# Kernel tuning notes

Hardware: AMD Instinct MI355X
Metric: run time of the kernel (lower is better)

The kernel has to match this reference:

```python
import jax, jax.numpy as jnp
import numpy as np

HIDDEN = 1024
BATCH = 32
SRC_LEN = 4096


def setup_inputs() -> dict:
    key = jax.random.key(0)
    k1, k2, k3, k4, k5 = jax.random.split(key, 5)
    query = jax.random.normal(k1, (BATCH, HIDDEN), dtype=jnp.float32)
    keys = jax.random.normal(k2, (BATCH, SRC_LEN, HIDDEN), dtype=jnp.float32)
    values = jax.random.normal(k3, (BATCH, SRC_LEN, HIDDEN), dtype=jnp.float32)
    mask = jax.random.randint(k4, (BATCH, SRC_LEN), 0, 2).astype(jnp.bool_)
    # nn.Linear(hidden, hidden, bias=False): y = x @ W.T, W: (out, in)
    W = jax.random.normal(k5, (HIDDEN, HIDDEN), dtype=jnp.float32) / np.sqrt(HIDDEN)
    return {"query": query, "keys": keys, "values": values, "mask": mask, "W": W}


def reference(query, keys, values, mask, W):
    # proj_query = linear_in(query): (b, h)
    proj_query = query @ W.T
    # scores = bmm(keys, proj_query[:, :, None]).squeeze: (b, s)
    scores = jnp.einsum("bsh,bh->bs", keys, proj_query)
    scores = jnp.where(mask, -jnp.inf, scores)
    attn_weights = jax.nn.softmax(scores, axis=-1)  # (b, s)
    # context = bmm(attn[:, None, :], values).squeeze: (b, h)
    context = jnp.einsum("bs,bsh->bh", attn_weights, values)
    return (context, attn_weights)
```

## Files before the change

kernel.cpp:

```cpp
#include <hip/hip_runtime.h>

constexpr int HIDDEN = 1024;
constexpr int BATCH  = 32;
constexpr int SRC    = 4096;
constexpr int CHUNK  = 128;
constexpr int NCHUNK = SRC / CHUNK;
constexpr int KSPLIT = 4;

#define NEG_INF (-__builtin_inff())


typedef float floatx4 __attribute__((ext_vector_type(4)));

__device__ __forceinline__ float4 ntload4(const float4* p) {
    floatx4 v = __builtin_nontemporal_load((const floatx4*)p);
    return make_float4(v.x, v.y, v.z, v.w);
}

__device__ __forceinline__ float wave_reduce_add(float v) {
    #pragma unroll
    for (int off = 32; off > 0; off >>= 1)
        v += __shfl_down(v, off, 64);
    return v;
}

__device__ __forceinline__ float wave_reduce_max(float v) {
    #pragma unroll
    for (int off = 32; off > 0; off >>= 1)
        v = fmaxf(v, __shfl_down(v, off, 64));
    return v;
}

__device__ __forceinline__ float dot16(float4 a, float4 b, float4 c, float4 d,
                                       float4 q0, float4 q1, float4 q2, float4 q3) {
    return a.x*q0.x + a.y*q0.y + a.z*q0.z + a.w*q0.w
         + b.x*q1.x + b.y*q1.y + b.z*q1.z + b.w*q1.w
         + c.x*q2.x + c.y*q2.y + c.z*q2.z + c.w*q2.w
         + d.x*q3.x + d.y*q3.y + d.z*q3.z + d.w*q3.w;
}

__global__ __launch_bounds__(256) void k_proj(const float* __restrict__ query,
                                              const float* __restrict__ W,
                                              float* __restrict__ pproj) {
    int g = blockIdx.x * 256 + threadIdx.x;
    int b = g & (BATCH - 1);
    int o = g >> 5;
    int z = blockIdx.y;
    const float4* W4 = (const float4*)(W + (size_t)o * HIDDEN) + z * (HIDDEN / 4 / KSPLIT);
    const float4* Q4 = (const float4*)(query + (size_t)b * HIDDEN) + z * (HIDDEN / 4 / KSPLIT);
    float4 acc = {0.f, 0.f, 0.f, 0.f};
    #pragma unroll 8
    for (int i = 0; i < HIDDEN / 4 / KSPLIT; ++i) {
        float4 w = W4[i];
        float4 q = Q4[i];
        acc.x += w.x * q.x; acc.y += w.y * q.y;
        acc.z += w.z * q.z; acc.w += w.w * q.w;
    }
    pproj[((size_t)z * BATCH + b) * HIDDEN + o] = acc.x + acc.y + acc.z + acc.w;
}

__global__ __launch_bounds__(256, 4) void k_fused(const float* __restrict__ keys,
                                                  const float* __restrict__ values,
                                                  const float* __restrict__ pproj,
                                                  const int* __restrict__ mask,
                                                  float* __restrict__ scores_out,
                                                  float* __restrict__ part,
                                                  float* __restrict__ lmax_arr,
                                                  float* __restrict__ lsum_arr) {
    int b   = blockIdx.x;
    int ch  = blockIdx.y;
    int tid = threadIdx.x;
    int wid = tid >> 6, lane = tid & 63;

    __shared__ float sc[CHUNK];
    __shared__ float red[8];
    __shared__ int   wcnt[2];
    __shared__ int   idxc[CHUNK];
    __shared__ float pwc[CHUNK];

    float4 q0, q1, q2, q3;
    {
        const float4* pz0 = (const float4*)(pproj + ((size_t)0 * BATCH + b) * HIDDEN);
        const float4* pz1 = (const float4*)(pproj + ((size_t)1 * BATCH + b) * HIDDEN);
        const float4* pz2 = (const float4*)(pproj + ((size_t)2 * BATCH + b) * HIDDEN);
        const float4* pz3 = (const float4*)(pproj + ((size_t)3 * BATCH + b) * HIDDEN);
        #pragma unroll
        for (int f = 0; f < 4; ++f) {
            int idx = lane + f * 64;
            float4 a = pz0[idx], bb = pz1[idx], c = pz2[idx], d = pz3[idx];
            float4 s;
            s.x = (a.x + bb.x) + (c.x + d.x);
            s.y = (a.y + bb.y) + (c.y + d.y);
            s.z = (a.z + bb.z) + (c.z + d.z);
            s.w = (a.w + bb.w) + (c.w + d.w);
            if (f == 0) q0 = s; else if (f == 1) q1 = s; else if (f == 2) q2 = s; else q3 = s;
        }
    }
    int s0    = ch * CHUNK;
    int rbase = wid * 32;

    int mrow = (lane < 32) ? mask[(size_t)b * SRC + s0 + rbase + lane] : 1;
    unsigned mbits = (unsigned)(__ballot(mrow != 0) & 0xffffffffull);

    #pragma unroll
    for (int h = 0; h < 2; ++h) {
        float acc[16];
        #pragma unroll 2
        for (int r = 0; r < 16; ++r) {
            int rr = h * 16 + r;
            if (!((mbits >> rr) & 1)) {
                const float4* krow =
                    (const float4*)(keys + ((size_t)b * SRC + s0 + rbase + rr) * HIDDEN);
                float4 a = ntload4(krow + lane);
                float4 c = ntload4(krow + lane + 64);
                float4 d = ntload4(krow + lane + 128);
                float4 e = ntload4(krow + lane + 192);
                acc[r] = dot16(a, c, d, e, q0, q1, q2, q3);
            } else {
                acc[r] = NEG_INF;
            }
        }
        #pragma unroll
        for (int r = 0; r < 16; ++r)
            if (!((mbits >> (h * 16 + r)) & 1)) acc[r] = wave_reduce_add(acc[r]);
        if (lane == 0) {
            #pragma unroll
            for (int r = 0; r < 16; ++r) {
                int row = rbase + h * 16 + r;
                sc[row] = acc[r];
                scores_out[(size_t)b * SRC + s0 + row] = acc[r];
            }
        }
    }
    __syncthreads();

    float myv = (tid < CHUNK) ? sc[tid] : NEG_INF;
    float wm = wave_reduce_max(myv);
    if (lane == 0) red[wid] = wm;
    __syncthreads();
    float lmax = fmaxf(fmaxf(red[0], red[1]), fmaxf(red[2], red[3]));

    float pe  = 0.f;
    bool live = false;
    if (tid < CHUNK) {
        pe   = (lmax == NEG_INF) ? 0.f : __expf(myv - lmax);
        live = (pe > 0.f);
    }
    unsigned long long bal = __ballot(live);
    int pos  = __popcll(bal & ((1ull << lane) - 1ull));
    int wtot = __popcll(bal);
    if (wid < 2 && lane == 0) wcnt[wid] = wtot;

    float ws = wave_reduce_add(pe);
    if (lane == 0) red[4 + wid] = ws;
    __syncthreads();

    if (live) {
        int base = (wid == 1) ? wcnt[0] : 0;
        idxc[base + pos] = tid;
        pwc [base + pos] = pe;
    }
    if (tid == 0) {
        lmax_arr[b * NCHUNK + ch] = lmax;
        lsum_arr[b * NCHUNK + ch] = red[4] + red[5] + red[6] + red[7];
    }
    __syncthreads();
    int cnt = wcnt[0] + wcnt[1];

    const float4* v4 = (const float4*)(values + ((size_t)b * SRC + s0) * HIDDEN);
    float4 acc = {0.f, 0.f, 0.f, 0.f};
    #pragma unroll 4
    for (int i = 0; i < cnt; ++i) {
        float  w   = pwc[i];
        int    row = idxc[i];
        float4 v   = ntload4(v4 + (size_t)row * 256 + tid);
        acc.x += w * v.x; acc.y += w * v.y; acc.z += w * v.z; acc.w += w * v.w;
    }
    ((float4*)(part + (size_t)(b * NCHUNK + ch) * HIDDEN))[tid] = acc;
}

__global__ __launch_bounds__(256) void k_combine(const float* __restrict__ part,
                                                 const float* __restrict__ lmax_arr,
                                                 const float* __restrict__ lsum_arr,
                                                 const float* __restrict__ scores,
                                                 float* __restrict__ ctx,
                                                 float* __restrict__ attn) {
    int b = blockIdx.x, y = blockIdx.y, tid = threadIdx.x;
    __shared__ float sm[NCHUNK], ss[NCHUNK];
    if (tid < NCHUNK) {
        sm[tid] = lmax_arr[b * NCHUNK + tid];
        ss[tid] = lsum_arr[b * NCHUNK + tid];
    }
    __syncthreads();

    float M = NEG_INF;
    #pragma unroll
    for (int c = 0; c < NCHUNK; ++c) M = fmaxf(M, sm[c]);
    float Sum = 0.f;
    #pragma unroll
    for (int c = 0; c < NCHUNK; ++c) {
        float e = (sm[c] == NEG_INF) ? 0.f : __expf(sm[c] - M);
        Sum += ss[c] * e;
    }
    float inv = 1.f / Sum;

    if (y == 0) {
        const float4* p4 = (const float4*)(part + (size_t)b * NCHUNK * HIDDEN);
        float4 acc = {0.f, 0.f, 0.f, 0.f};
        #pragma unroll
        for (int c = 0; c < NCHUNK; ++c) {
            float w = ((sm[c] == NEG_INF) ? 0.f : __expf(sm[c] - M)) * inv;
            float4 v = p4[c * 256 + tid];
            acc.x += w * v.x; acc.y += w * v.y; acc.z += w * v.z; acc.w += w * v.w;
        }
        ((float4*)(ctx + (size_t)b * HIDDEN))[tid] = acc;
    } else {
        int base = (y - 1) * (SRC / 16);
        const float4* s4 = (const float4*)(scores + (size_t)b * SRC);
        float4*       a4 = (float4*)(attn + (size_t)b * SRC);
        float4 v = s4[base + tid];
        float4 r;
        r.x = __expf(v.x - M) * inv;
        r.y = __expf(v.y - M) * inv;
        r.z = __expf(v.z - M) * inv;
        r.w = __expf(v.w - M) * inv;
        a4[base + tid] = r;
    }
}

extern "C" void kernel_launch(void* const* d_in, const int* in_sizes, int n_in,
                              void* d_out, int out_size, void* d_ws, size_t ws_size,
                              hipStream_t stream) {
    const float* query  = (const float*)d_in[0];
    const float* keys   = (const float*)d_in[1];
    const float* values = (const float*)d_in[2];
    const int*   mask   = (const int*)d_in[3];
    const float* W      = (const float*)d_in[4];

    float* ctx  = (float*)d_out;
    float* attn = (float*)d_out + BATCH * HIDDEN;

    float* pproj  = (float*)d_ws;
    float* scores = pproj + (size_t)KSPLIT * BATCH * HIDDEN;
    float* part   = scores + BATCH * SRC;
    float* lmax   = part + (size_t)BATCH * NCHUNK * HIDDEN;
    float* lsum   = lmax + BATCH * NCHUNK;

    k_proj   <<<dim3(BATCH * HIDDEN / 256, KSPLIT), 256, 0, stream>>>(query, W, pproj);
    k_fused  <<<dim3(BATCH, NCHUNK),                256, 0, stream>>>(keys, values, pproj, mask,
                                                                      scores, part, lmax, lsum);
    k_combine<<<dim3(BATCH, 5),                     256, 0, stream>>>(part, lmax, lsum, scores,
                                                                      ctx, attn);
}
```

Measured before the change: 102.0 us.

## Fuse combine kernel into fused kernel via last-block atomic counter

```diff
diff --git a/kernel.cpp b/kernel.cpp
--- a/kernel.cpp
+++ b/kernel.cpp
@@ -41,7 +41,10 @@
 
 __global__ __launch_bounds__(256) void k_proj(const float* __restrict__ query,
                                               const float* __restrict__ W,
-                                              float* __restrict__ pproj) {
+                                              float* __restrict__ pproj,
+                                              int* __restrict__ counter) {
+    if (blockIdx.x == 0 && blockIdx.y == 0 && threadIdx.x < BATCH)
+        counter[threadIdx.x] = 0;
     int g = blockIdx.x * 256 + threadIdx.x;
     int b = g & (BATCH - 1);
     int o = g >> 5;
@@ -66,7 +69,10 @@
                                                   float* __restrict__ scores_out,
                                                   float* __restrict__ part,
                                                   float* __restrict__ lmax_arr,
-                                                  float* __restrict__ lsum_arr) {
+                                                  float* __restrict__ lsum_arr,
+                                                  int* __restrict__ counter,
+                                                  float* __restrict__ ctx,
+                                                  float* __restrict__ attn) {
     int b   = blockIdx.x;
     int ch  = blockIdx.y;
     int tid = threadIdx.x;
@@ -77,6 +83,7 @@
     __shared__ int   wcnt[2];
     __shared__ int   idxc[CHUNK];
     __shared__ float pwc[CHUNK];
+    __shared__ int   is_last;
 
     float4 q0, q1, q2, q3;
     {
@@ -177,15 +184,17 @@
         acc.x += w * v.x; acc.y += w * v.y; acc.z += w * v.z; acc.w += w * v.w;
     }
     ((float4*)(part + (size_t)(b * NCHUNK + ch) * HIDDEN))[tid] = acc;
-}
-
-__global__ __launch_bounds__(256) void k_combine(const float* __restrict__ part,
-                                                 const float* __restrict__ lmax_arr,
-                                                 const float* __restrict__ lsum_arr,
-                                                 const float* __restrict__ scores,
-                                                 float* __restrict__ ctx,
-                                                 float* __restrict__ attn) {
-    int b = blockIdx.x, y = blockIdx.y, tid = threadIdx.x;
+
+    __syncthreads();
+    if (tid == 0) {
+        __threadfence();
+        int old = atomicAdd(&counter[b], 1);
+        is_last = (old == NCHUNK - 1) ? 1 : 0;
+    }
+    __syncthreads();
+    if (!is_last) return;
+    __threadfence();
+
     __shared__ float sm[NCHUNK], ss[NCHUNK];
     if (tid < NCHUNK) {
         sm[tid] = lmax_arr[b * NCHUNK + tid];
@@ -204,27 +213,27 @@
     }
     float inv = 1.f / Sum;
 
-    if (y == 0) {
-        const float4* p4 = (const float4*)(part + (size_t)b * NCHUNK * HIDDEN);
-        float4 acc = {0.f, 0.f, 0.f, 0.f};
-        #pragma unroll
-        for (int c = 0; c < NCHUNK; ++c) {
-            float w = ((sm[c] == NEG_INF) ? 0.f : __expf(sm[c] - M)) * inv;
-            float4 v = p4[c * 256 + tid];
-            acc.x += w * v.x; acc.y += w * v.y; acc.z += w * v.z; acc.w += w * v.w;
-        }
-        ((float4*)(ctx + (size_t)b * HIDDEN))[tid] = acc;
-    } else {
-        int base = (y - 1) * (SRC / 16);
-        const float4* s4 = (const float4*)(scores + (size_t)b * SRC);
-        float4*       a4 = (float4*)(attn + (size_t)b * SRC);
-        float4 v = s4[base + tid];
+    const float4* p4 = (const float4*)(part + (size_t)b * NCHUNK * HIDDEN);
+    float4 cacc = {0.f, 0.f, 0.f, 0.f};
+    #pragma unroll
+    for (int c = 0; c < NCHUNK; ++c) {
+        float w = ((sm[c] == NEG_INF) ? 0.f : __expf(sm[c] - M)) * inv;
+        float4 v = p4[c * 256 + tid];
+        cacc.x += w * v.x; cacc.y += w * v.y; cacc.z += w * v.z; cacc.w += w * v.w;
+    }
+    ((float4*)(ctx + (size_t)b * HIDDEN))[tid] = cacc;
+
+    const float4* s4 = (const float4*)(scores_out + (size_t)b * SRC);
+    float4*       a4 = (float4*)(attn + (size_t)b * SRC);
+    #pragma unroll
+    for (int j = tid; j < SRC / 4; j += 256) {
+        float4 v = s4[j];
         float4 r;
         r.x = __expf(v.x - M) * inv;
         r.y = __expf(v.y - M) * inv;
         r.z = __expf(v.z - M) * inv;
         r.w = __expf(v.w - M) * inv;
-        a4[base + tid] = r;
+        a4[j] = r;
     }
 }
 
@@ -245,10 +254,10 @@
     float* part   = scores + BATCH * SRC;
     float* lmax   = part + (size_t)BATCH * NCHUNK * HIDDEN;
     float* lsum   = lmax + BATCH * NCHUNK;
-
-    k_proj   <<<dim3(BATCH * HIDDEN / 256, KSPLIT), 256, 0, stream>>>(query, W, pproj);
-    k_fused  <<<dim3(BATCH, NCHUNK),                256, 0, stream>>>(keys, values, pproj, mask,
-                                                                      scores, part, lmax, lsum);
-    k_combine<<<dim3(BATCH, 5),                     256, 0, stream>>>(part, lmax, lsum, scores,
-                                                                      ctx, attn);
-}
+    int*   counter = (int*)(lsum + BATCH * NCHUNK);
+
+    k_proj <<<dim3(BATCH * HIDDEN / 256, KSPLIT), 256, 0, stream>>>(query, W, pproj, counter);
+    k_fused<<<dim3(BATCH, NCHUNK),                256, 0, stream>>>(keys, values, pproj, mask,
+                                                                    scores, part, lmax, lsum,
+                                                                    counter, ctx, attn);
+}
```

Result: slower. 151.0 us (+48.0%).
